# Performance work log

Hardware: AMD Instinct MI355X
Metric: run time of the kernel (lower is better)

## Reference

```python
import jax, jax.numpy as jnp
import numpy as np
import math

B, L, H, E, D = 4, 2048, 8, 64, 64
EPS = 1e-6

def _adjust(x):
    # signed power-law (sqrt) then L2-normalize over feature dim
    y = jnp.sign(x) * jnp.sqrt(jnp.abs(x) + EPS)
    return y / (jnp.linalg.norm(y, axis=-1, keepdims=True) + EPS)

def setup_inputs() -> dict:
    key = jax.random.key(0)
    kq, kk, kv, ka = jax.random.split(key, 4)
    queries = jax.random.normal(kq, (B, L, H, E), dtype=jnp.float32)
    keys = jax.random.normal(kk, (B, L, H, E), dtype=jnp.float32)
    values = jax.random.normal(kv, (B, L, H, D), dtype=jnp.float32)
    # TriangularCausalMask: True above the diagonal => masked
    attn_mask = jnp.triu(jnp.ones((1, 1, L, L), dtype=bool), k=1)
    alpha = jax.random.normal(ka, (1,), dtype=jnp.float32) * 0.01
    return {"queries": queries, "keys": keys, "values": values,
            "attn_mask": attn_mask, "alpha": alpha}

def reference(queries, keys, values, attn_mask, alpha):
    Bq, Lq, Hq, Eq = queries.shape
    scale = 1.0 / math.sqrt(Eq)
    # Closed form of torch.autograd.functional.jacobian of
    # sum(einsum('blhe,bshe->bhls', q, k)):
    #   d/dq[b,l,h,e] = sum_s k[b,s,h,e]   (independent of l)
    #   d/dk[b,s,h,e] = sum_l q[b,l,h,e]   (independent of s)
    k_sum = jnp.sum(keys, axis=1, keepdims=True)      # [B,1,H,E]
    q_sum = jnp.sum(queries, axis=1, keepdims=True)   # [B,1,H,E]
    q_adj = _adjust(queries + alpha * k_sum)
    k_adj = _adjust(keys + alpha * q_sum)
    scores = jnp.einsum('blhe,bshe->bhls', q_adj, k_adj)  # [B,H,L,S]
    scores = jnp.where(attn_mask, -jnp.inf, scores)
    A = jax.nn.softmax(scale * scores, axis=-1)  # dropout inactive (eval)
    V = jnp.einsum('bhls,bshd->blhd', A, values)
    return V
```

## Files before the change

kernel.cpp:

```cpp
#include <hip/hip_runtime.h>
#include <hip/hip_bf16.h>
#include <math.h>

#define NB 4
#define NL 2048
#define NH 8
#define NE 64
#define ND 64
#define EPSF 1e-6f
#define CEXP 0.180336881f

typedef __attribute__((ext_vector_type(8))) short bf16x8;
typedef __attribute__((ext_vector_type(4))) short s16x4;
typedef __attribute__((ext_vector_type(4))) float f32x4;

static __device__ __forceinline__ unsigned short bfbits(float x) {
  union { __hip_bfloat16 h; unsigned short u; } c;
  c.h = __float2bfloat16(x);
  return c.u;
}
static __device__ __forceinline__ float sgnsqrt(float x) {
  return x > 0.f ? sqrtf(x + EPSF) : (x < 0.f ? -sqrtf(-x + EPSF) : 0.f);
}

__global__ void sums_kernel(const float* __restrict__ q, const float* __restrict__ k,
                            float* __restrict__ pq, float* __restrict__ pk) {
  int bh = blockIdx.x, lp = blockIdx.y;
  int b = bh >> 3, h = bh & 7;
  int t = threadIdx.x;
  int eq = t & 15, lr = t >> 4;
  int wave = t >> 6, lane = t & 63;
  const float* qp = q + (((size_t)b * NL) * NH + h) * NE + eq * 4;
  const float* kp = k + (((size_t)b * NL) * NH + h) * NE + eq * 4;
  f32x4 aq = {0.f, 0.f, 0.f, 0.f}, ak = {0.f, 0.f, 0.f, 0.f};
#pragma unroll
  for (int i = 0; i < 8; ++i) {
    int l = lp * 128 + i * 16 + lr;
    size_t off = (size_t)l * NH * NE;
    aq += *(const f32x4*)(qp + off);
    ak += *(const f32x4*)(kp + off);
  }
#pragma unroll
  for (int c = 0; c < 4; ++c) {
    aq[c] += __shfl_xor(aq[c], 16, 64); aq[c] += __shfl_xor(aq[c], 32, 64);
    ak[c] += __shfl_xor(ak[c], 16, 64); ak[c] += __shfl_xor(ak[c], 32, 64);
  }
  __shared__ f32x4 sq[4][16], sk[4][16];
  if (lane < 16) { sq[wave][lane] = aq; sk[wave][lane] = ak; }
  __syncthreads();
  if (t < 16) {
    f32x4 s = sq[0][t] + sq[1][t] + sq[2][t] + sq[3][t];
    *(f32x4*)(pq + ((size_t)bh * 16 + lp) * 64 + t * 4) = s;
  } else if (t < 32) {
    int e = t - 16;
    f32x4 s = sk[0][e] + sk[1][e] + sk[2][e] + sk[3][e];
    *(f32x4*)(pk + ((size_t)bh * 16 + lp) * 64 + e * 4) = s;
  }
}

__global__ void prep_kernel(const float* __restrict__ q, const float* __restrict__ k,
                            const float* __restrict__ v,
                            const float* __restrict__ pq, const float* __restrict__ pk,
                            const float* __restrict__ alpha,
                            __hip_bfloat16* __restrict__ qadj, __hip_bfloat16* __restrict__ kadj,
                            __hip_bfloat16* __restrict__ vt) {
  __shared__ float aqs[8][68], aks[8][68];
  __shared__ __hip_bfloat16 tile[64][68];
  int t = threadIdx.x;
  if (blockIdx.x < 1024) {
    int rid0 = blockIdx.x * 64;
    int b = rid0 >> 14;
    {
      int h = t >> 5, j = t & 31;
      const float* pqp = pq + ((size_t)(b * 8 + h) * 16) * 64 + j * 2;
      const float* pkp = pk + ((size_t)(b * 8 + h) * 16) * 64 + j * 2;
      float s0 = 0.f, s1 = 0.f, u0 = 0.f, u1 = 0.f;
#pragma unroll
      for (int lp = 0; lp < 16; ++lp) {
        s0 += pqp[lp * 64]; s1 += pqp[lp * 64 + 1];
        u0 += pkp[lp * 64]; u1 += pkp[lp * 64 + 1];
      }
      float al = alpha[0];
      aqs[h][j * 2] = al * s0; aqs[h][j * 2 + 1] = al * s1;
      aks[h][j * 2] = al * u0; aks[h][j * 2 + 1] = al * u1;
    }
    __syncthreads();
    int eq = t & 15, lr = t >> 4;
#pragma unroll
    for (int p = 0; p < 4; ++p) {
      int rid = rid0 + p * 16 + lr;
      int h = rid & 7, l = (rid >> 3) & 2047;
      f32x4 q4 = *(const f32x4*)(q + (size_t)rid * 64 + eq * 4);
      f32x4 k4 = *(const f32x4*)(k + (size_t)rid * 64 + eq * 4);
      f32x4 xq = q4 + *(const f32x4*)&aks[h][eq * 4];
      f32x4 xk = k4 + *(const f32x4*)&aqs[h][eq * 4];
      float yq[4], yk[4];
      float nq = 0.f, nk = 0.f;
#pragma unroll
      for (int c = 0; c < 4; ++c) {
        yq[c] = sgnsqrt(xq[c]); nq += yq[c] * yq[c];
        yk[c] = sgnsqrt(xk[c]); nk += yk[c] * yk[c];
      }
#pragma unroll
      for (int m = 1; m < 16; m <<= 1) {
        nq += __shfl_xor(nq, m, 16);
        nk += __shfl_xor(nk, m, 16);
      }
      float iq = 1.f / (sqrtf(nq) + EPSF);
      float ik = 1.f / (sqrtf(nk) + EPSF);
      s16x4 uq, uk;
#pragma unroll
      for (int c = 0; c < 4; ++c) {
        uq[c] = (short)bfbits(yq[c] * iq);
        uk[c] = (short)bfbits(yk[c] * ik);
      }
      size_t ooff = ((size_t)(b * 8 + h) * 2048 + l) * 64 + eq * 4;
      *(s16x4*)((char*)qadj + ooff * 2) = uq;
      *(s16x4*)((char*)kadj + ooff * 2) = uk;
    }
  } else {
    int blk = blockIdx.x - 1024;
    int s0 = (blk & 31) * 64;
    int bh = blk >> 5;
    int b = bh >> 3, h = bh & 7;
    {
      int sl = t >> 2, dg = t & 3;
      const float* src = v + (((size_t)b * NL + s0 + sl) * NH + h) * ND + dg * 16;
#pragma unroll
      for (int i = 0; i < 4; ++i) {
        f32x4 f = *(const f32x4*)(src + i * 4);
        tile[sl][dg * 16 + i * 4 + 0] = __float2bfloat16(f[0]);
        tile[sl][dg * 16 + i * 4 + 1] = __float2bfloat16(f[1]);
        tile[sl][dg * 16 + i * 4 + 2] = __float2bfloat16(f[2]);
        tile[sl][dg * 16 + i * 4 + 3] = __float2bfloat16(f[3]);
      }
    }
    __syncthreads();
    {
      int d = t >> 2, sg = t & 3;
      __align__(16) __hip_bfloat16 tmp[16];
#pragma unroll
      for (int i = 0; i < 16; ++i) {
        int c = sg * 16 + i;
        int blk32 = c >> 5, cc = c & 31;
        int cq = cc >> 2, ege = cq >> 1, hi = cq & 1;
        int s_local = blk32 * 32 + hi * 16 + ege * 4 + (cc & 3);
        tmp[i] = tile[s_local][d];
      }
      __hip_bfloat16* dst = vt + ((size_t)bh * ND + d) * NL + s0 + sg * 16;
      *(bf16x8*)(dst) = *(const bf16x8*)&tmp[0];
      *(bf16x8*)(dst + 8) = *(const bf16x8*)&tmp[8];
    }
  }
}

__global__ __launch_bounds__(256, 5) void attn_kernel(const __hip_bfloat16* __restrict__ qadj,
                                                      const __hip_bfloat16* __restrict__ kadj,
                                                      const __hip_bfloat16* __restrict__ vt,
                                                      float* __restrict__ out) {
  __shared__ __align__(16) char lds[32768];
  int bh = blockIdx.x;
  int tile = 63 - (int)blockIdx.y;
  int b = bh >> 3, h = bh & 7;
  int wave = threadIdx.x >> 6, lane = threadIdx.x & 63;
  int qr = lane & 15, eg = lane >> 4;
  int qhalf = wave >> 1, shalf = wave & 1;
  int t0 = tile * 32;
  int nck = (tile >> 1) + 1;
  int qw0 = t0 + qhalf * 16;
  const char* kgb = (const char*)(kadj + (size_t)bh * NL * NE);
  const char* vgb = (const char*)(vt + (size_t)bh * ND * NL);
  const char* qgb = (const char*)(qadj + (size_t)bh * NL * NE);

  int koff[2][2], voff[4];
#pragma unroll
  for (int st2 = 0; st2 < 2; ++st2) {
    int row = shalf * 32 + st2 * 16 + qr;
    int swz = (row & 7) << 4;
    koff[st2][0] = (row * 128 + eg * 16) ^ swz;
    koff[st2][1] = (row * 128 + 64 + eg * 16) ^ swz;
  }
#pragma unroll
  for (int dc = 0; dc < 4; ++dc) {
    int d = dc * 16 + qr;
    voff[dc] = 8192 + ((d * 128 + shalf * 64 + eg * 16) ^ ((d & 7) << 4));
  }
  int src_off[4], dst_off[4];
#pragma unroll
  for (int c = 0; c < 4; ++c) {
    dst_off[c] = (wave * 4 + c) * 1024;
    if (wave < 2) {
      int T = (wave * 4 + c) * 1024 + lane * 16;
      src_off[c] = T ^ (((T >> 7) & 7) << 4);
    } else {
      int T2 = ((wave - 2) * 4 + c) * 1024 + lane * 16;
      int S = T2 ^ (((T2 >> 7) & 7) << 4);
      src_off[c] = (S >> 7) * (NL * 2) + (S & 127);
    }
  }
  const char* sgb = (wave < 2) ? kgb : vgb;
  int smul = (wave < 2) ? 8192 : 128;

  auto STAGE = [&](int bufsel, int ck) {
    const char* sb = sgb + (size_t)ck * smul;
    char* db = lds + bufsel * 16384;
#pragma unroll
    for (int c = 0; c < 4; ++c)
      __builtin_amdgcn_global_load_lds(
          (const __attribute__((address_space(1))) unsigned int*)(sb + src_off[c]),
          (__attribute__((address_space(3))) unsigned int*)(db + dst_off[c]),
          16, 0, 0);
  };

  bf16x8 qf0 = *(const bf16x8*)(qgb + (size_t)(qw0 + qr) * 128 + eg * 16);
  bf16x8 qf1 = *(const bf16x8*)(qgb + (size_t)(qw0 + qr) * 128 + 64 + eg * 16);

  f32x4 acc[4];
#pragma unroll
  for (int dc = 0; dc < 4; ++dc) acc[dc] = (f32x4){0.f, 0.f, 0.f, 0.f};
  float srun = 0.f;

  STAGE(0, 0);
#pragma unroll 1
  for (int ck = 0; ck < nck; ++ck) {
    asm volatile("s_waitcnt vmcnt(0)" ::: "memory");
    __builtin_amdgcn_sched_barrier(0);
    __builtin_amdgcn_s_barrier();
    __builtin_amdgcn_sched_barrier(0);
    if (ck + 1 < nck) STAGE((ck + 1) & 1, ck + 1);
    char* base = lds + (ck & 1) * 16384;

    float p[2][4];
#pragma unroll
    for (int st2 = 0; st2 < 2; ++st2) {
      f32x4 a = (f32x4){0.f, 0.f, 0.f, 0.f};
      bf16x8 k0 = *(const bf16x8*)(base + koff[st2][0]);
      bf16x8 k1 = *(const bf16x8*)(base + koff[st2][1]);
      a = __builtin_amdgcn_mfma_f32_16x16x32_bf16(k0, qf0, a, 0, 0, 0);
      a = __builtin_amdgcn_mfma_f32_16x16x32_bf16(k1, qf1, a, 0, 0, 0);
#pragma unroll
      for (int r = 0; r < 4; ++r) p[st2][r] = a[r];
    }
    if (ck == nck - 1) {
      int sbase = ck * 64 + shalf * 32 + eg * 4;
      int qg = qw0 + qr;
#pragma unroll
      for (int st2 = 0; st2 < 2; ++st2)
#pragma unroll
        for (int r = 0; r < 4; ++r)
          if (sbase + st2 * 16 + r > qg) p[st2][r] = -1e30f;
    }
#pragma unroll
    for (int st2 = 0; st2 < 2; ++st2)
#pragma unroll
      for (int r = 0; r < 4; ++r) p[st2][r] = exp2f((p[st2][r] - 1.0f) * CEXP);
    srun += ((p[0][0] + p[0][1]) + (p[0][2] + p[0][3])) +
            ((p[1][0] + p[1][1]) + (p[1][2] + p[1][3]));

    bf16x8 pb;
#pragma unroll
    for (int j = 0; j < 4; ++j) {
      pb[j] = (short)bfbits(p[0][j]);
      pb[4 + j] = (short)bfbits(p[1][j]);
    }
#pragma unroll
    for (int dc = 0; dc < 4; ++dc) {
      bf16x8 vf = *(const bf16x8*)(base + voff[dc]);
      acc[dc] = __builtin_amdgcn_mfma_f32_16x16x32_bf16(vf, pb, acc[dc], 0, 0, 0);
    }
  }

  srun += __shfl_xor(srun, 16, 64);
  srun += __shfl_xor(srun, 32, 64);
  __syncthreads();
  if (shalf == 1) {
    float* m = (float*)(lds + qhalf * 4352 + lane * 68);
#pragma unroll
    for (int dc = 0; dc < 4; ++dc)
#pragma unroll
      for (int r = 0; r < 4; ++r) m[dc * 4 + r] = acc[dc][r];
    m[16] = srun;
  }
  __syncthreads();
  if (shalf == 0) {
    const float* m = (const float*)(lds + qhalf * 4352 + lane * 68);
#pragma unroll
    for (int dc = 0; dc < 4; ++dc)
#pragma unroll
      for (int r = 0; r < 4; ++r) acc[dc][r] += m[dc * 4 + r];
    float inv = 1.f / (srun + m[16]);
    int l = qw0 + qr;
    float* orow = out + (((size_t)b * NL + l) * NH + h) * ND;
#pragma unroll
    for (int dc = 0; dc < 4; ++dc) *(f32x4*)(orow + dc * 16 + eg * 4) = acc[dc] * inv;
  }
}

extern "C" void kernel_launch(void* const* d_in, const int* in_sizes, int n_in,
                              void* d_out, int out_size, void* d_ws, size_t ws_size,
                              hipStream_t stream) {
  const float* q = (const float*)d_in[0];
  const float* k = (const float*)d_in[1];
  const float* v = (const float*)d_in[2];
  const float* alpha = (const float*)d_in[4];
  float* out = (float*)d_out;
  char* ws = (char*)d_ws;

  __hip_bfloat16* qadj = (__hip_bfloat16*)(ws);
  __hip_bfloat16* kadj = (__hip_bfloat16*)(ws + 8388608);
  __hip_bfloat16* vt   = (__hip_bfloat16*)(ws + 16777216);
  float* pq = (float*)(ws + 25165824);
  float* pk = (float*)(ws + 25165824 + 131072);

  sums_kernel<<<dim3(32, 16), 256, 0, stream>>>(q, k, pq, pk);
  prep_kernel<<<dim3(2048), 256, 0, stream>>>(q, k, v, pq, pk, alpha, qadj, kadj, vt);
  attn_kernel<<<dim3(32, 64), 256, 0, stream>>>(qadj, kadj, vt, out);
}
```

Before: 151.7 us.

## Fuse sums and prep into cooperative kernel; triple-buffer attention K/V staging

Result: slower. 542.2 us (+257.4%).

```diff
diff --git a/kernel.cpp b/kernel.cpp
--- a/kernel.cpp
+++ b/kernel.cpp
@@ -1,6 +1,9 @@
 #include <hip/hip_runtime.h>
 #include <hip/hip_bf16.h>
+#include <hip/hip_cooperative_groups.h>
 #include <math.h>
+
+namespace cg = cooperative_groups;
 
 #define NB 4
 #define NL 2048
@@ -23,77 +26,123 @@
   return x > 0.f ? sqrtf(x + EPSF) : (x < 0.f ? -sqrtf(-x + EPSF) : 0.f);
 }
 
-__global__ void sums_kernel(const float* __restrict__ q, const float* __restrict__ k,
-                            float* __restrict__ pq, float* __restrict__ pk) {
-  int bh = blockIdx.x, lp = blockIdx.y;
-  int b = bh >> 3, h = bh & 7;
+__global__ __launch_bounds__(256, 4) void prep_kernel(
+    const float* __restrict__ q, const float* __restrict__ k, const float* __restrict__ v,
+    const float* __restrict__ alpha,
+    float* __restrict__ pq, float* __restrict__ pk,
+    float* __restrict__ qsumT, float* __restrict__ ksumT,
+    __hip_bfloat16* __restrict__ qadj, __hip_bfloat16* __restrict__ kadj,
+    __hip_bfloat16* __restrict__ vt) {
+  __shared__ __align__(16) char sh[16384];
+  cg::grid_group grid = cg::this_grid();
+  int blk = blockIdx.x;
   int t = threadIdx.x;
-  int eq = t & 15, lr = t >> 4;
-  int wave = t >> 6, lane = t & 63;
-  const float* qp = q + (((size_t)b * NL) * NH + h) * NE + eq * 4;
-  const float* kp = k + (((size_t)b * NL) * NH + h) * NE + eq * 4;
-  f32x4 aq = {0.f, 0.f, 0.f, 0.f}, ak = {0.f, 0.f, 0.f, 0.f};
-#pragma unroll
-  for (int i = 0; i < 8; ++i) {
-    int l = lp * 128 + i * 16 + lr;
-    size_t off = (size_t)l * NH * NE;
-    aq += *(const f32x4*)(qp + off);
-    ak += *(const f32x4*)(kp + off);
-  }
-#pragma unroll
-  for (int c = 0; c < 4; ++c) {
-    aq[c] += __shfl_xor(aq[c], 16, 64); aq[c] += __shfl_xor(aq[c], 32, 64);
-    ak[c] += __shfl_xor(ak[c], 16, 64); ak[c] += __shfl_xor(ak[c], 32, 64);
-  }
-  __shared__ f32x4 sq[4][16], sk[4][16];
-  if (lane < 16) { sq[wave][lane] = aq; sk[wave][lane] = ak; }
-  __syncthreads();
-  if (t < 16) {
-    f32x4 s = sq[0][t] + sq[1][t] + sq[2][t] + sq[3][t];
-    *(f32x4*)(pq + ((size_t)bh * 16 + lp) * 64 + t * 4) = s;
-  } else if (t < 32) {
-    int e = t - 16;
-    f32x4 s = sk[0][e] + sk[1][e] + sk[2][e] + sk[3][e];
-    *(f32x4*)(pk + ((size_t)bh * 16 + lp) * 64 + e * 4) = s;
-  }
-}
-
-__global__ void prep_kernel(const float* __restrict__ q, const float* __restrict__ k,
-                            const float* __restrict__ v,
-                            const float* __restrict__ pq, const float* __restrict__ pk,
-                            const float* __restrict__ alpha,
-                            __hip_bfloat16* __restrict__ qadj, __hip_bfloat16* __restrict__ kadj,
-                            __hip_bfloat16* __restrict__ vt) {
-  __shared__ float aqs[8][68], aks[8][68];
-  __shared__ __hip_bfloat16 tile[64][68];
-  int t = threadIdx.x;
-  if (blockIdx.x < 1024) {
-    int rid0 = blockIdx.x * 64;
-    int b = rid0 >> 14;
-    {
-      int h = t >> 5, j = t & 31;
-      const float* pqp = pq + ((size_t)(b * 8 + h) * 16) * 64 + j * 2;
-      const float* pkp = pk + ((size_t)(b * 8 + h) * 16) * 64 + j * 2;
-      float s0 = 0.f, s1 = 0.f, u0 = 0.f, u1 = 0.f;
-#pragma unroll
-      for (int lp = 0; lp < 16; ++lp) {
-        s0 += pqp[lp * 64]; s1 += pqp[lp * 64 + 1];
-        u0 += pkp[lp * 64]; u1 += pkp[lp * 64 + 1];
-      }
-      float al = alpha[0];
-      aqs[h][j * 2] = al * s0; aqs[h][j * 2 + 1] = al * s1;
-      aks[h][j * 2] = al * u0; aks[h][j * 2 + 1] = al * u1;
-    }
-    __syncthreads();
-    int eq = t & 15, lr = t >> 4;
-#pragma unroll
-    for (int p = 0; p < 4; ++p) {
-      int rid = rid0 + p * 16 + lr;
-      int h = rid & 7, l = (rid >> 3) & 2047;
-      f32x4 q4 = *(const f32x4*)(q + (size_t)rid * 64 + eq * 4);
-      f32x4 k4 = *(const f32x4*)(k + (size_t)rid * 64 + eq * 4);
-      f32x4 xq = q4 + *(const f32x4*)&aks[h][eq * 4];
-      f32x4 xk = k4 + *(const f32x4*)&aqs[h][eq * 4];
+  int b = blk >> 8;
+  int col4 = t & 15;
+
+  int rid0 = blk * 64;
+  f32x4 q4[4], k4[4];
+#pragma unroll
+  for (int j = 0; j < 4; ++j) {
+    size_t off = ((size_t)(rid0 + (t >> 4) + 16 * j) * 64 + col4 * 4);
+    q4[j] = *(const f32x4*)(q + off);
+    k4[j] = *(const f32x4*)(k + off);
+  }
+  {
+    f32x4* arr = (f32x4*)sh;
+    f32x4 ps = (q4[0] + q4[1]) + (q4[2] + q4[3]);
+    arr[t] = ps;
+    __syncthreads();
+    if (t < 128) {
+      f32x4 tot = arr[t] + arr[t + 128];
+      int h = (t >> 4) & 7;
+      *(f32x4*)(pq + (size_t)blk * 512 + h * 64 + col4 * 4) = tot;
+    }
+    __syncthreads();
+    ps = (k4[0] + k4[1]) + (k4[2] + k4[3]);
+    arr[t] = ps;
+    __syncthreads();
+    if (t < 128) {
+      f32x4 tot = arr[t] + arr[t + 128];
+      int h = (t >> 4) & 7;
+      *(f32x4*)(pk + (size_t)blk * 512 + h * 64 + col4 * 4) = tot;
+    }
+    __syncthreads();
+  }
+  {
+    __hip_bfloat16 (*tile)[68] = (__hip_bfloat16(*)[68])(sh + 4096);
+    int vbh = blk >> 5, s0 = (blk & 31) * 64;
+    int vb = vbh >> 3, vh = vbh & 7;
+    int sl = t >> 2, dg = t & 3;
+    const float* src = v + (((size_t)vb * NL + s0 + sl) * NH + vh) * ND + dg * 16;
+#pragma unroll
+    for (int i = 0; i < 4; ++i) {
+      f32x4 f = *(const f32x4*)(src + i * 4);
+      tile[sl][dg * 16 + i * 4 + 0] = __float2bfloat16(f[0]);
+      tile[sl][dg * 16 + i * 4 + 1] = __float2bfloat16(f[1]);
+      tile[sl][dg * 16 + i * 4 + 2] = __float2bfloat16(f[2]);
+      tile[sl][dg * 16 + i * 4 + 3] = __float2bfloat16(f[3]);
+    }
+    __syncthreads();
+    int d = t >> 2, sg = t & 3;
+    __align__(16) __hip_bfloat16 tmp[16];
+#pragma unroll
+    for (int i = 0; i < 16; ++i) {
+      int c = sg * 16 + i;
+      int blk32 = c >> 5, cc = c & 31;
+      int cq = cc >> 2, ege = cq >> 1, hi = cq & 1;
+      int s_local = blk32 * 32 + hi * 16 + ege * 4 + (cc & 3);
+      tmp[i] = tile[s_local][d];
+    }
+    __hip_bfloat16* dst = vt + ((size_t)vbh * ND + d) * NL + s0 + sg * 16;
+    *(bf16x8*)(dst) = *(const bf16x8*)&tmp[0];
+    *(bf16x8*)(dst + 8) = *(const bf16x8*)&tmp[8];
+  }
+
+  __threadfence();
+  grid.sync();
+
+  if (blk < 32) {
+    int rb = blk >> 3, rh = blk & 7;
+    int e = t & 63, g = t >> 6;
+    float* red = (float*)sh;
+    float sq = 0.f, sk = 0.f;
+    for (int i = 0; i < 64; ++i) {
+      size_t sb = (size_t)(rb * 256 + g + 4 * i) * 512 + rh * 64 + e;
+      sq += pq[sb];
+      sk += pk[sb];
+    }
+    red[g * 64 + e] = sq;
+    red[256 + g * 64 + e] = sk;
+    __syncthreads();
+    if (t < 64) {
+      qsumT[blk * 64 + t] = red[t] + red[64 + t] + red[128 + t] + red[192 + t];
+      ksumT[blk * 64 + t] = red[256 + t] + red[320 + t] + red[384 + t] + red[448 + t];
+    }
+  }
+
+  __threadfence();
+  grid.sync();
+
+  {
+    float* tabq = (float*)sh;
+    float* tabk = (float*)(sh + 2048);
+    float al = alpha[0];
+    if (t < 128) {
+      f32x4 a = *(const f32x4*)(qsumT + b * 512 + t * 4);
+      f32x4 c = *(const f32x4*)(ksumT + b * 512 + t * 4);
+      *(f32x4*)(tabq + t * 4) = a * al;
+      *(f32x4*)(tabk + t * 4) = c * al;
+    }
+    __syncthreads();
+    int h = (t >> 4) & 7;
+    f32x4 aq = *(const f32x4*)(tabk + h * 64 + col4 * 4);
+    f32x4 ak = *(const f32x4*)(tabq + h * 64 + col4 * 4);
+    int bh = b * 8 + h;
+#pragma unroll
+    for (int j = 0; j < 4; ++j) {
+      f32x4 xq = q4[j] + aq;
+      f32x4 xk = k4[j] + ak;
       float yq[4], yk[4];
       float nq = 0.f, nk = 0.f;
 #pragma unroll
@@ -114,51 +163,19 @@
         uq[c] = (short)bfbits(yq[c] * iq);
         uk[c] = (short)bfbits(yk[c] * ik);
       }
-      size_t ooff = ((size_t)(b * 8 + h) * 2048 + l) * 64 + eq * 4;
+      int l = (blk & 255) * 8 + (t >> 7) + 2 * j;
+      size_t ooff = ((size_t)bh * 2048 + l) * 64 + col4 * 4;
       *(s16x4*)((char*)qadj + ooff * 2) = uq;
       *(s16x4*)((char*)kadj + ooff * 2) = uk;
     }
-  } else {
-    int blk = blockIdx.x - 1024;
-    int s0 = (blk & 31) * 64;
-    int bh = blk >> 5;
-    int b = bh >> 3, h = bh & 7;
-    {
-      int sl = t >> 2, dg = t & 3;
-      const float* src = v + (((size_t)b * NL + s0 + sl) * NH + h) * ND + dg * 16;
-#pragma unroll
-      for (int i = 0; i < 4; ++i) {
-        f32x4 f = *(const f32x4*)(src + i * 4);
-        tile[sl][dg * 16 + i * 4 + 0] = __float2bfloat16(f[0]);
-        tile[sl][dg * 16 + i * 4 + 1] = __float2bfloat16(f[1]);
-        tile[sl][dg * 16 + i * 4 + 2] = __float2bfloat16(f[2]);
-        tile[sl][dg * 16 + i * 4 + 3] = __float2bfloat16(f[3]);
-      }
-    }
-    __syncthreads();
-    {
-      int d = t >> 2, sg = t & 3;
-      __align__(16) __hip_bfloat16 tmp[16];
-#pragma unroll
-      for (int i = 0; i < 16; ++i) {
-        int c = sg * 16 + i;
-        int blk32 = c >> 5, cc = c & 31;
-        int cq = cc >> 2, ege = cq >> 1, hi = cq & 1;
-        int s_local = blk32 * 32 + hi * 16 + ege * 4 + (cc & 3);
-        tmp[i] = tile[s_local][d];
-      }
-      __hip_bfloat16* dst = vt + ((size_t)bh * ND + d) * NL + s0 + sg * 16;
-      *(bf16x8*)(dst) = *(const bf16x8*)&tmp[0];
-      *(bf16x8*)(dst + 8) = *(const bf16x8*)&tmp[8];
-    }
-  }
-}
-
-__global__ __launch_bounds__(256, 5) void attn_kernel(const __hip_bfloat16* __restrict__ qadj,
+  }
+}
+
+__global__ __launch_bounds__(256, 3) void attn_kernel(const __hip_bfloat16* __restrict__ qadj,
                                                       const __hip_bfloat16* __restrict__ kadj,
                                                       const __hip_bfloat16* __restrict__ vt,
                                                       float* __restrict__ out) {
-  __shared__ __align__(16) char lds[32768];
+  __shared__ __align__(16) char lds[49152];
   int bh = blockIdx.x;
   int tile = 63 - (int)blockIdx.y;
   int b = bh >> 3, h = bh & 7;
@@ -201,9 +218,9 @@
   const char* sgb = (wave < 2) ? kgb : vgb;
   int smul = (wave < 2) ? 8192 : 128;
 
-  auto STAGE = [&](int bufsel, int ck) {
+  auto STAGE = [&](int bufoff, int ck) {
     const char* sb = sgb + (size_t)ck * smul;
-    char* db = lds + bufsel * 16384;
+    char* db = lds + bufoff;
 #pragma unroll
     for (int c = 0; c < 4; ++c)
       __builtin_amdgcn_global_load_lds(
@@ -221,16 +238,22 @@
   float srun = 0.f;
 
   STAGE(0, 0);
+  if (nck > 1) STAGE(16384, 1);
+
+  int off_c = 0;
+  int off_s = 32768;
 #pragma unroll 1
   for (int ck = 0; ck < nck; ++ck) {
-    asm volatile("s_waitcnt vmcnt(0)" ::: "memory");
+    if (ck + 1 < nck) asm volatile("s_waitcnt vmcnt(4)" ::: "memory");
+    else              asm volatile("s_waitcnt vmcnt(0)" ::: "memory");
     __builtin_amdgcn_sched_barrier(0);
     __builtin_amdgcn_s_barrier();
     __builtin_amdgcn_sched_barrier(0);
-    if (ck + 1 < nck) STAGE((ck + 1) & 1, ck + 1);
-    char* base = lds + (ck & 1) * 16384;
+    if (ck + 2 < nck) STAGE(off_s, ck + 2);
+    char* base = lds + off_c;
 
     float p[2][4];
+    __builtin_amdgcn_s_setprio(1);
 #pragma unroll
     for (int st2 = 0; st2 < 2; ++st2) {
       f32x4 a = (f32x4){0.f, 0.f, 0.f, 0.f};
@@ -241,6 +264,7 @@
 #pragma unroll
       for (int r = 0; r < 4; ++r) p[st2][r] = a[r];
     }
+    __builtin_amdgcn_s_setprio(0);
     if (ck == nck - 1) {
       int sbase = ck * 64 + shalf * 32 + eg * 4;
       int qg = qw0 + qr;
@@ -263,11 +287,16 @@
       pb[j] = (short)bfbits(p[0][j]);
       pb[4 + j] = (short)bfbits(p[1][j]);
     }
+    __builtin_amdgcn_s_setprio(1);
 #pragma unroll
     for (int dc = 0; dc < 4; ++dc) {
       bf16x8 vf = *(const bf16x8*)(base + voff[dc]);
       acc[dc] = __builtin_amdgcn_mfma_f32_16x16x32_bf16(vf, pb, acc[dc], 0, 0, 0);
     }
+    __builtin_amdgcn_s_setprio(0);
+
+    off_c = (off_c == 32768) ? 0 : off_c + 16384;
+    off_s = (off_s == 32768) ? 0 : off_s + 16384;
   }
 
   srun += __shfl_xor(srun, 16, 64);
@@ -309,10 +338,15 @@
   __hip_bfloat16* qadj = (__hip_bfloat16*)(ws);
   __hip_bfloat16* kadj = (__hip_bfloat16*)(ws + 8388608);
   __hip_bfloat16* vt   = (__hip_bfloat16*)(ws + 16777216);
-  float* pq = (float*)(ws + 25165824);
-  float* pk = (float*)(ws + 25165824 + 131072);
-
-  sums_kernel<<<dim3(32, 16), 256, 0, stream>>>(q, k, pq, pk);
-  prep_kernel<<<dim3(2048), 256, 0, stream>>>(q, k, v, pq, pk, alpha, qadj, kadj, vt);
+  float* pq    = (float*)(ws + 25165824);
+  float* pk    = (float*)(ws + 25165824 + 2097152);
+  float* qsumT = (float*)(ws + 25165824 + 4194304);
+  float* ksumT = (float*)(ws + 25165824 + 4194304 + 8192);
+
+  void* args[] = {(void*)&q, (void*)&k, (void*)&v, (void*)&alpha,
+                  (void*)&pq, (void*)&pk, (void*)&qsumT, (void*)&ksumT,
+                  (void*)&qadj, (void*)&kadj, (void*)&vt};
+  hipLaunchCooperativeKernel((const void*)prep_kernel, dim3(1024), dim3(256),
+                             args, 0, stream);
   attn_kernel<<<dim3(32, 64), 256, 0, stream>>>(qadj, kadj, vt, out);
 }
```
